# Optimization experiments

Hardware: AMD Instinct MI355X
Metric: run time of the kernel (lower is better)

The kernel has to match this reference:

```python
import jax, jax.numpy as jnp
import numpy as np

SHAPES = ((80, 80), (40, 40), (20, 20), (10, 10))  # (H, W) per level
N_HEADS = 8
N_POINTS = 4
D_MODEL = 512  # double_d_model = 2*256 (densefusion=True)
D_FFN = 1024
B = 2
L = len(SHAPES)
S = sum(h * w for h, w in SHAPES)  # 8500
EPS = 1e-5


def _layernorm(x, g, b):
    m = jnp.mean(x, axis=-1, keepdims=True)
    v = jnp.mean((x - m) ** 2, axis=-1, keepdims=True)
    return (x - m) * jax.lax.rsqrt(v + EPS) * g + b


def _reference_points(shapes):
    # encoder get_reference_points with valid_ratios == 1 -> [S, 2] (x, y) in (0,1)
    refs = []
    for (H, W) in shapes:
        ry = (jnp.arange(H, dtype=jnp.float32) + 0.5) / H
        rx = (jnp.arange(W, dtype=jnp.float32) + 0.5) / W
        gy, gx = jnp.meshgrid(ry, rx, indexing='ij')
        refs.append(jnp.stack([gx.reshape(-1), gy.reshape(-1)], axis=-1))
    return jnp.concatenate(refs, axis=0)


def _sample_level(val, loc, H, W):
    # val: [B, H*W, h, d]; loc: [B, S, h, P, 2] normalized in [0,1]
    b, _, h, d = val.shape
    s, p = loc.shape[1], loc.shape[3]
    x = loc[..., 0] * W - 0.5
    y = loc[..., 1] * H - 0.5
    x0 = jnp.floor(x)
    y0 = jnp.floor(y)
    wx = x - x0
    wy = y - y0
    x0i = x0.astype(jnp.int32)
    y0i = y0.astype(jnp.int32)

    def gather(xi, yi):
        valid = ((xi >= 0) & (xi < W) & (yi >= 0) & (yi < H)).astype(val.dtype)
        idx = jnp.clip(yi, 0, H - 1) * W + jnp.clip(xi, 0, W - 1)  # [B,S,h,P]
        idx2 = jnp.transpose(idx, (0, 1, 3, 2)).reshape(b, s * p, h)  # [B,S*P,h]
        g = jnp.take_along_axis(val, idx2[..., None], axis=1)  # [B,S*P,h,d]
        vmask = jnp.transpose(valid, (0, 1, 3, 2))[..., None]  # [B,S,P,h,1]
        return g.reshape(b, s, p, h, d) * vmask

    v00 = gather(x0i, y0i)
    v01 = gather(x0i + 1, y0i)
    v10 = gather(x0i, y0i + 1)
    v11 = gather(x0i + 1, y0i + 1)
    wxT = jnp.transpose(wx, (0, 1, 3, 2))[..., None]
    wyT = jnp.transpose(wy, (0, 1, 3, 2))[..., None]
    return (v00 * (1 - wxT) * (1 - wyT) + v01 * wxT * (1 - wyT)
            + v10 * (1 - wxT) * wyT + v11 * wxT * wyT)  # [B,S,P,h,d]


def _forward(src, pos, w_off, b_off, w_attn, b_attn, w_val, b_val, w_out, b_out,
             ln1_g, ln1_b, w1, b1, w2, b2, ln2_g, ln2_b, shapes):
    b, s, c = src.shape
    h, p, l = N_HEADS, N_POINTS, len(shapes)
    d = c // h
    q = src + pos
    value = (src @ w_val + b_val).reshape(b, s, h, d)
    offsets = (q @ w_off + b_off).reshape(b, s, h, l, p, 2)
    attn = jax.nn.softmax((q @ w_attn + b_attn).reshape(b, s, h, l * p), axis=-1)
    attn = attn.reshape(b, s, h, l, p)
    ref = _reference_points(shapes)  # [S,2]
    # offset normalizer = (W_l, H_l)
    norm = jnp.array([[W, H] for (H, W) in shapes], dtype=src.dtype)  # [L,2]
    loc = ref[None, :, None, None, None, :] + offsets / norm[None, None, None, :, None, :]
    # split value per level and sample
    starts = np.cumsum([0] + [H * W for (H, W) in shapes])[:-1]
    sampled = []
    for lvl, (H, W) in enumerate(shapes):
        val_l = jax.lax.dynamic_slice_in_dim(value, int(starts[lvl]), H * W, axis=1)
        sampled.append(_sample_level(val_l, loc[:, :, :, lvl], H, W))
    sampled = jnp.stack(sampled)  # [L,B,S,P,h,d]
    out = jnp.einsum('lbqphd,bqhlp->bqhd', sampled, attn).reshape(b, s, c)
    attn_out = out @ w_out + b_out
    x = _layernorm(src + attn_out, ln1_g, ln1_b)
    ffn = jax.nn.relu(x @ w1 + b1) @ w2 + b2
    return _layernorm(x + ffn, ln2_g, ln2_b)


def setup_inputs() -> dict:
    key = jax.random.key(0)
    ks = jax.random.split(key, 20)
    sc = 0.02
    C = D_MODEL
    hLP = N_HEADS * L * N_POINTS
    f32 = jnp.float32
    inp = {
        'src': jax.random.normal(ks[0], (B, S, C), f32),
        'pos': jax.random.normal(ks[1], (B, S, C), f32),
        'w_off': jax.random.normal(ks[2], (C, hLP * 2), f32) * sc,
        'b_off': jax.random.normal(ks[3], (hLP * 2,), f32) * sc,
        'w_attn': jax.random.normal(ks[4], (C, hLP), f32) * sc,
        'b_attn': jax.random.normal(ks[5], (hLP,), f32) * sc,
        'w_val': jax.random.normal(ks[6], (C, C), f32) * sc,
        'b_val': jnp.zeros((C,), f32),
        'w_out': jax.random.normal(ks[7], (C, C), f32) * sc,
        'b_out': jnp.zeros((C,), f32),
        'ln1_g': jnp.ones((C,), f32),
        'ln1_b': jnp.zeros((C,), f32),
        'w1': jax.random.normal(ks[8], (C, D_FFN), f32) * sc,
        'b1': jnp.zeros((D_FFN,), f32),
        'w2': jax.random.normal(ks[9], (D_FFN, C), f32) * sc,
        'b2': jnp.zeros((C,), f32),
        'ln2_g': jnp.ones((C,), f32),
        'ln2_b': jnp.zeros((C,), f32),
        'spatial_shapes': jnp.array(SHAPES, dtype=jnp.int32),
    }
    return inp


def reference(src, pos, w_off, b_off, w_attn, b_attn, w_val, b_val, w_out, b_out,
              ln1_g, ln1_b, w1, b1, w2, b2, ln2_g, ln2_b, spatial_shapes):
    shapes = tuple((int(a), int(b)) for a, b in np.asarray(spatial_shapes))
    return _forward(src, pos, w_off, b_off, w_attn, b_attn, w_val, b_val, w_out, b_out,
                    ln1_g, ln1_b, w1, b1, w2, b2, ln2_g, ln2_b, shapes)
```

## Files before the change

kernel.cpp:

```cpp
#include <hip/hip_runtime.h>


typedef __bf16 bf16_t;
typedef __bf16 bf16x8 __attribute__((ext_vector_type(8)));
typedef __bf16 bf16x4 __attribute__((ext_vector_type(4)));
typedef float  f32x2  __attribute__((ext_vector_type(2)));
typedef float  f32x4  __attribute__((ext_vector_type(4)));
typedef float  f32x16 __attribute__((ext_vector_type(16)));

#define M_ROWS 17000
#define S_LEN  8500

__device__ inline void store_c(float* p, float v)  { *p = v; }
__device__ inline void store_c(bf16_t* p, float v) { *p = (bf16_t)v; }

__device__ inline float4 load4f(const float* p)  { return *(const float4*)p; }
__device__ inline float4 load4f(const bf16_t* p) {
    bf16x4 v = *(const bf16x4*)p;
    return make_float4((float)v[0], (float)v[1], (float)v[2], (float)v[3]);
}

__device__ inline void pk_fma(f32x2& a, f32x2 x, f32x2 y) {
    asm("v_pk_fma_f32 %0, %1, %2, %0" : "+v"(a) : "v"(x), "v"(y));
}

__global__ __launch_bounds__(256)
void prep_kernel(const float* __restrict__ w_val, const float* __restrict__ w_off,
                 const float* __restrict__ w_attn, const float* __restrict__ w_out,
                 const float* __restrict__ w1, const float* __restrict__ w2,
                 const float* __restrict__ b_off, const float* __restrict__ b_attn,
                 bf16_t* __restrict__ wt_val, bf16_t* __restrict__ wt_oa,
                 bf16_t* __restrict__ wt_out, bf16_t* __restrict__ wt_w1,
                 bf16_t* __restrict__ wt_w2, float* __restrict__ bias_oa) {
    int z = blockIdx.z;
    if (z == 6) {
        if (blockIdx.x == 0 && blockIdx.y == 0) {
            for (int i = threadIdx.x; i < 384; i += 256)
                bias_oa[i] = (i < 256) ? b_off[i] : b_attn[i - 256];
        }
        return;
    }
    const float* in; bf16_t* out; int K, N;
    switch (z) {
        case 0: in = w_val;  out = wt_val;                     K = 512;  N = 512;  break;
        case 1: in = w_off;  out = wt_oa;                      K = 512;  N = 256;  break;
        case 2: in = w_attn; out = wt_oa + (size_t)256 * 512;  K = 512;  N = 128;  break;
        case 3: in = w_out;  out = wt_out;                     K = 512;  N = 512;  break;
        case 4: in = w1;     out = wt_w1;                      K = 512;  N = 1024; break;
        default: in = w2;    out = wt_w2;                      K = 1024; N = 512;  break;
    }
    int k0 = blockIdx.x * 32, n0 = blockIdx.y * 32;
    if (k0 >= K || n0 >= N) return;
    __shared__ float s[32][33];
    int tx = threadIdx.x & 31, ty = threadIdx.x >> 5;
    #pragma unroll
    for (int i = 0; i < 4; i++)
        s[ty + 8 * i][tx] = in[(size_t)(k0 + ty + 8 * i) * N + n0 + tx];
    __syncthreads();
    #pragma unroll
    for (int i = 0; i < 4; i++)
        out[(size_t)(n0 + ty + 8 * i) * K + k0 + tx] = (bf16_t)s[tx][ty + 8 * i];
}

__global__ __launch_bounds__(256)
void add_q_kernel(const float* __restrict__ a, const float* __restrict__ b,
                  bf16_t* __restrict__ q, bf16_t* __restrict__ src_bf, int n4) {
    int i = blockIdx.x * 256 + threadIdx.x;
    if (i >= n4) return;
    float4 av = *(const float4*)(a + (size_t)i * 4);
    float4 bv = *(const float4*)(b + (size_t)i * 4);
    bf16x4 sv, ov;
    sv[0] = (bf16_t)av.x; sv[1] = (bf16_t)av.y; sv[2] = (bf16_t)av.z; sv[3] = (bf16_t)av.w;
    ov[0] = (bf16_t)(av.x + bv.x);
    ov[1] = (bf16_t)(av.y + bv.y);
    ov[2] = (bf16_t)(av.z + bv.z);
    ov[3] = (bf16_t)(av.w + bv.w);
    *(bf16x4*)(q      + (size_t)i * 4) = ov;
    *(bf16x4*)(src_bf + (size_t)i * 4) = sv;
}

#define GEMM_CORE(A_PTR, WT_PTR, K_DIM, EPILOGUE)                                  \
    const int tid  = threadIdx.x;                                                  \
    const int wave = tid >> 6;                                                     \
    const int lane = tid & 63;                                                     \
    const int l31  = lane & 31;                                                    \
    const int lh8  = (lane >> 5) * 8;                                              \
    const int wr   = (wave >> 1) * 64;                                             \
    const int wc   = (wave & 1) * 64;                                              \
    const int row0 = blockIdx.x * 128;                                             \
    const int sr = tid >> 2;                                                       \
    const int sc = (tid & 3) * 8;                                                  \
    const bf16_t* gA0 = A_PTR  + (size_t)min(row0 + sr,      M_ROWS - 1) * K_DIM + sc; \
    const bf16_t* gA1 = A_PTR  + (size_t)min(row0 + sr + 64, M_ROWS - 1) * K_DIM + sc; \
    const bf16_t* gB0 = WT_PTR + (size_t)(col0 + sr) * K_DIM + sc;                 \
    const bf16_t* gB1 = WT_PTR + (size_t)(col0 + sr + 64) * K_DIM + sc;            \
    f32x16 acc[2][2];                                                              \
    _Pragma("unroll")                                                              \
    for (int i = 0; i < 2; i++)                                                    \
        _Pragma("unroll")                                                          \
        for (int j = 0; j < 2; j++)                                                \
            _Pragma("unroll")                                                      \
            for (int r = 0; r < 16; r++) acc[i][j][r] = 0.f;                       \
    bf16x8 pa0 = *(const bf16x8*)gA0;                                              \
    bf16x8 pa1 = *(const bf16x8*)gA1;                                              \
    bf16x8 pb0 = *(const bf16x8*)gB0;                                              \
    bf16x8 pb1 = *(const bf16x8*)gB1;                                              \
    const int nIter = K_DIM >> 5;                                                  \
    for (int it = 0; it < nIter; it++) {                                           \
        const int cur = it & 1;                                                    \
        *(bf16x8*)&As[cur][sr][sc]      = pa0;                                     \
        *(bf16x8*)&As[cur][sr + 64][sc] = pa1;                                     \
        *(bf16x8*)&Bs[cur][sr][sc]      = pb0;                                     \
        *(bf16x8*)&Bs[cur][sr + 64][sc] = pb1;                                     \
        __syncthreads();                                                           \
        if (it + 1 < nIter) {                                                      \
            int ko = (it + 1) << 5;                                                \
            pa0 = *(const bf16x8*)(gA0 + ko);                                      \
            pa1 = *(const bf16x8*)(gA1 + ko);                                      \
            pb0 = *(const bf16x8*)(gB0 + ko);                                      \
            pb1 = *(const bf16x8*)(gB1 + ko);                                      \
        }                                                                          \
        _Pragma("unroll")                                                          \
        for (int kh = 0; kh < 2; kh++) {                                           \
            bf16x8 a0 = *(const bf16x8*)&As[cur][wr + l31     ][kh * 16 + lh8];    \
            bf16x8 a1 = *(const bf16x8*)&As[cur][wr + 32 + l31][kh * 16 + lh8];    \
            bf16x8 b0 = *(const bf16x8*)&Bs[cur][wc + l31     ][kh * 16 + lh8];    \
            bf16x8 b1 = *(const bf16x8*)&Bs[cur][wc + 32 + l31][kh * 16 + lh8];    \
            acc[0][0] = __builtin_amdgcn_mfma_f32_32x32x16_bf16(a0, b0, acc[0][0], 0, 0, 0); \
            acc[0][1] = __builtin_amdgcn_mfma_f32_32x32x16_bf16(a0, b1, acc[0][1], 0, 0, 0); \
            acc[1][0] = __builtin_amdgcn_mfma_f32_32x32x16_bf16(a1, b0, acc[1][0], 0, 0, 0); \
            acc[1][1] = __builtin_amdgcn_mfma_f32_32x32x16_bf16(a1, b1, acc[1][1], 0, 0, 0); \
        }                                                                          \
    }                                                                              \
    EPILOGUE

template<typename OT, bool RELU>
__global__ __launch_bounds__(256)
void gemm128_kernel(const bf16_t* __restrict__ A, const bf16_t* __restrict__ Wt,
                    const float* __restrict__ bias, OT* __restrict__ Cout,
                    int N, int K) {
    __shared__ bf16_t As[2][128][40];
    __shared__ bf16_t Bs[2][128][40];
    const int col0 = blockIdx.y * 128;
    GEMM_CORE(A, Wt, K,
        {
            _Pragma("unroll")
            for (int i = 0; i < 2; i++)
                _Pragma("unroll")
                for (int j = 0; j < 2; j++) {
                    int col = col0 + wc + j * 32 + l31;
                    float bcol = bias[col];
                    _Pragma("unroll")
                    for (int reg = 0; reg < 16; reg++) {
                        int row = row0 + wr + i * 32 + (reg & 3) + 8 * (reg >> 2) + 4 * (lane >> 5);
                        if (row < M_ROWS) {
                            float v = acc[i][j][reg] + bcol;
                            if (RELU) v = fmaxf(v, 0.f);
                            store_c(Cout + (size_t)row * N + col, v);
                        }
                    }
                }
        }
    )
}

__global__ __launch_bounds__(256)
void gemm_voa_kernel(const bf16_t* __restrict__ src_bf, const bf16_t* __restrict__ q,
                     const bf16_t* __restrict__ wt_val, const bf16_t* __restrict__ wt_oa,
                     const float* __restrict__ b_val, const float* __restrict__ bias_oa,
                     bf16_t* __restrict__ value, float* __restrict__ oa) {
    __shared__ bf16_t As[2][128][40];
    __shared__ bf16_t Bs[2][128][40];
    const int by    = blockIdx.y;
    const bool isV  = by < 4;
    const int col0  = (isV ? by : by - 4) * 128;
    const bf16_t* Ap  = isV ? src_bf : q;
    const bf16_t* Wp  = isV ? wt_val : wt_oa;
    const float* bp   = isV ? b_val : bias_oa;
    GEMM_CORE(Ap, Wp, 512,
        {
            _Pragma("unroll")
            for (int i = 0; i < 2; i++)
                _Pragma("unroll")
                for (int j = 0; j < 2; j++) {
                    int col = col0 + wc + j * 32 + l31;
                    float bcol = bp[col];
                    _Pragma("unroll")
                    for (int reg = 0; reg < 16; reg++) {
                        int row = row0 + wr + i * 32 + (reg & 3) + 8 * (reg >> 2) + 4 * (lane >> 5);
                        if (row < M_ROWS) {
                            float v = acc[i][j][reg] + bcol;
                            if (isV) value[(size_t)row * 512 + col] = (bf16_t)v;
                            else     oa[(size_t)row * 384 + col] = v;
                        }
                    }
                }
        }
    )
}

__global__ __launch_bounds__(256)
void sample_kernel(const bf16_t* __restrict__ value, const float* __restrict__ oa,
                   bf16_t* __restrict__ out) {
    __shared__ __align__(16) int sAW[4][2][8][68];
    const int wave = threadIdx.x >> 6;
    const int lane = threadIdx.x & 63;
    const int h    = lane >> 3;
    const int sub  = lane & 7;
    const int bs   = blockIdx.x * 4 + wave;
    const int b    = bs / S_LEN;
    const int s    = bs - b * S_LEN;

    float rx, ry;
    if (s < 6400)      { int i = s;        const float inv = 1.f/80.f; ry = ((i/80) + 0.5f)*inv; rx = ((i%80) + 0.5f)*inv; }
    else if (s < 8000) { int i = s - 6400; const float inv = 1.f/40.f; ry = ((i/40) + 0.5f)*inv; rx = ((i%40) + 0.5f)*inv; }
    else if (s < 8400) { int i = s - 8000; const float inv = 1.f/20.f; ry = ((i/20) + 0.5f)*inv; rx = ((i%20) + 0.5f)*inv; }
    else               { int i = s - 8400; const float inv = 1.f/10.f; ry = ((i/10) + 0.5f)*inv; rx = ((i%10) + 0.5f)*inv; }

    const int WH[4]  = {80, 40, 20, 10};
    const int LST[4] = {0, 6400, 8000, 8400};
    const int ll = sub >> 1;
    const int W  = WH[ll];
    const int LS = LST[ll];

    const float* row = oa + (size_t)bs * 384;
    float4 o4 = *(const float4*)(row + h * 32 + sub * 4);
    float2 lg = *(const float2*)(row + 256 + h * 16 + sub * 2);

    float mx = fmaxf(lg.x, lg.y);
    mx = fmaxf(mx, __shfl_xor(mx, 1, 64));
    mx = fmaxf(mx, __shfl_xor(mx, 2, 64));
    mx = fmaxf(mx, __shfl_xor(mx, 4, 64));
    float e0 = __expf(lg.x - mx), e1 = __expf(lg.y - mx);
    float sm = e0 + e1;
    sm += __shfl_xor(sm, 1, 64);
    sm += __shfl_xor(sm, 2, 64);
    sm += __shfl_xor(sm, 4, 64);
    float pinv = 1.f / sm;

    #pragma unroll
    for (int t = 0; t < 2; t++) {
        float ox = t ? o4.z : o4.x;
        float oy = t ? o4.w : o4.y;
        float p  = (t ? e1 : e0) * pinv;
        float x = fmaf(rx, (float)W, ox) - 0.5f;
        float y = fmaf(ry, (float)W, oy) - 0.5f;
        float fx = floorf(x), fy = floorf(y);
        float wx = x - fx, wy = y - fy;
        int ix = (int)fx, iy = (int)fy;
        #pragma unroll
        for (int k2 = 0; k2 < 4; k2++) {
            int cx = ix + (k2 & 1);
            int cy = iy + (k2 >> 1);
            float wgt = p * ((k2 & 1) ? wx : 1.f - wx) * ((k2 >> 1) ? wy : 1.f - wy);
            if (cx < 0 || cx >= W || cy < 0 || cy >= W) wgt = 0.f;
            int xc = min(max(cx, 0), W - 1);
            int yc = min(max(cy, 0), W - 1);
            int c = sub * 8 + t * 4 + k2;
            sAW[wave][0][h][c] = LS + yc * W + xc;
            sAW[wave][1][h][c] = __float_as_int(wgt);
        }
    }
    __syncthreads();

    const bf16_t* vb = value + ((size_t)b * S_LEN) * 512 + h * 64 + sub * 8;
    f32x2 a01 = {0.f, 0.f}, a23 = {0.f, 0.f}, a45 = {0.f, 0.f}, a67 = {0.f, 0.f};

    #define ACC8(V, WW) {                                                          \
        f32x2 ws; ws[0] = (WW); ws[1] = (WW);                                      \
        f32x2 pv;                                                                  \
        pv[0] = __uint_as_float((V).x << 16);                                      \
        pv[1] = __uint_as_float((V).x & 0xffff0000u); pk_fma(a01, pv, ws);         \
        pv[0] = __uint_as_float((V).y << 16);                                      \
        pv[1] = __uint_as_float((V).y & 0xffff0000u); pk_fma(a23, pv, ws);         \
        pv[0] = __uint_as_float((V).z << 16);                                      \
        pv[1] = __uint_as_float((V).z & 0xffff0000u); pk_fma(a45, pv, ws);         \
        pv[0] = __uint_as_float((V).w << 16);                                      \
        pv[1] = __uint_as_float((V).w & 0xffff0000u); pk_fma(a67, pv, ws); }

    #pragma unroll 2
    for (int c8 = 0; c8 < 64; c8 += 8) {
        int4   ia = *(const int4*)  &sAW[wave][0][h][c8];
        int4   ib = *(const int4*)  &sAW[wave][0][h][c8 + 4];
        float4 wa = *(const float4*)&sAW[wave][1][h][c8];
        float4 wb = *(const float4*)&sAW[wave][1][h][c8 + 4];
        uint4 v0 = *(const uint4*)(vb + (size_t)ia.x * 512);
        uint4 v1 = *(const uint4*)(vb + (size_t)ia.y * 512);
        uint4 v2 = *(const uint4*)(vb + (size_t)ia.z * 512);
        uint4 v3 = *(const uint4*)(vb + (size_t)ia.w * 512);
        uint4 v4 = *(const uint4*)(vb + (size_t)ib.x * 512);
        uint4 v5 = *(const uint4*)(vb + (size_t)ib.y * 512);
        uint4 v6 = *(const uint4*)(vb + (size_t)ib.z * 512);
        uint4 v7 = *(const uint4*)(vb + (size_t)ib.w * 512);
        ACC8(v0, wa.x) ACC8(v1, wa.y) ACC8(v2, wa.z) ACC8(v3, wa.w)
        ACC8(v4, wb.x) ACC8(v5, wb.y) ACC8(v6, wb.z) ACC8(v7, wb.w)
    }
    #undef ACC8

    bf16x8 ov;
    ov[0] = (bf16_t)a01[0]; ov[1] = (bf16_t)a01[1];
    ov[2] = (bf16_t)a23[0]; ov[3] = (bf16_t)a23[1];
    ov[4] = (bf16_t)a45[0]; ov[5] = (bf16_t)a45[1];
    ov[6] = (bf16_t)a67[0]; ov[7] = (bf16_t)a67[1];
    *(bf16x8*)(out + (size_t)bs * 512 + h * 64 + sub * 8) = ov;
}

template<typename INA, typename INB, typename OT>
__global__ __launch_bounds__(256)
void ln_kernel(const INA* __restrict__ Xa, const INB* __restrict__ Xb,
               const float* __restrict__ g, const float* __restrict__ be,
               OT* __restrict__ out, int M) {
    int wave = threadIdx.x >> 6;
    int lane = threadIdx.x & 63;
    int row = blockIdx.x * 4 + wave;
    if (row >= M) return;
    size_t base = (size_t)row * 512;
    float v[8];
    float s = 0.f, sq = 0.f;
    #pragma unroll
    for (int p = 0; p < 2; p++) {
        int idx = p * 256 + lane * 4;
        float4 a4 = load4f(Xa + base + idx);
        float4 b4 = load4f(Xb + base + idx);
        float t0 = a4.x + b4.x, t1 = a4.y + b4.y, t2 = a4.z + b4.z, t3 = a4.w + b4.w;
        v[p*4+0] = t0; v[p*4+1] = t1; v[p*4+2] = t2; v[p*4+3] = t3;
        s  += t0 + t1 + t2 + t3;
        sq += t0*t0 + t1*t1 + t2*t2 + t3*t3;
    }
    #pragma unroll
    for (int off = 32; off > 0; off >>= 1) {
        s  += __shfl_xor(s, off, 64);
        sq += __shfl_xor(sq, off, 64);
    }
    float mean = s * (1.f / 512.f);
    float var  = sq * (1.f / 512.f) - mean * mean;
    float rstd = rsqrtf(var + 1e-5f);
    #pragma unroll
    for (int p = 0; p < 2; p++) {
        int idx = p * 256 + lane * 4;
        #pragma unroll
        for (int j = 0; j < 4; j++) {
            int col = idx + j;
            float o = (v[p*4+j] - mean) * rstd * g[col] + be[col];
            store_c(out + base + col, o);
        }
    }
}

extern "C" void kernel_launch(void* const* d_in, const int* in_sizes, int n_in,
                              void* d_out, int out_size, void* d_ws, size_t ws_size,
                              hipStream_t stream) {
    const float* src    = (const float*)d_in[0];
    const float* pos    = (const float*)d_in[1];
    const float* w_off  = (const float*)d_in[2];
    const float* b_off  = (const float*)d_in[3];
    const float* w_attn = (const float*)d_in[4];
    const float* b_attn = (const float*)d_in[5];
    const float* w_val  = (const float*)d_in[6];
    const float* b_val  = (const float*)d_in[7];
    const float* w_out  = (const float*)d_in[8];
    const float* b_out  = (const float*)d_in[9];
    const float* ln1_g  = (const float*)d_in[10];
    const float* ln1_b  = (const float*)d_in[11];
    const float* w1     = (const float*)d_in[12];
    const float* b1     = (const float*)d_in[13];
    const float* w2     = (const float*)d_in[14];
    const float* b2     = (const float*)d_in[15];
    const float* ln2_g  = (const float*)d_in[16];
    const float* ln2_b  = (const float*)d_in[17];

    const int M = M_ROWS;
    char* ws = (char*)d_ws;
    size_t o = 0;
    auto alloc = [&](size_t bytes) { size_t r = o; o += (bytes + 255) & ~(size_t)255; return r; };

    size_t off_q       = alloc((size_t)M * 512 * 2);
    size_t off_srcbf   = alloc((size_t)M * 512 * 2);
    size_t off_value   = alloc((size_t)M * 512 * 2);
    size_t off_sampled = alloc((size_t)M * 512 * 2);
    size_t off_oa      = alloc((size_t)M * 384 * 4);
    size_t off_attnout = alloc((size_t)M * 512 * 2);
    size_t off_x       = alloc((size_t)M * 512 * 2);
    size_t off_wtval   = alloc((size_t)512 * 512 * 2);
    size_t off_wtoa    = alloc((size_t)384 * 512 * 2);
    size_t off_wtout   = alloc((size_t)512 * 512 * 2);
    size_t off_wtw1    = alloc((size_t)1024 * 512 * 2);
    size_t off_wtw2    = alloc((size_t)512 * 1024 * 2);
    size_t off_boa     = alloc((size_t)384 * 4);

    bf16_t* q        = (bf16_t*)(ws + off_q);
    bf16_t* src_bf   = (bf16_t*)(ws + off_srcbf);
    bf16_t* value    = (bf16_t*)(ws + off_value);
    bf16_t* sampled  = (bf16_t*)(ws + off_sampled);
    float*  oa       = (float*)(ws + off_oa);
    bf16_t* attn_out = (bf16_t*)(ws + off_attnout);
    bf16_t* x        = (bf16_t*)(ws + off_x);
    bf16_t* hidden   = (bf16_t*)(ws + off_sampled);
    bf16_t* ffn_out  = (bf16_t*)(ws + off_attnout);
    bf16_t* wt_val   = (bf16_t*)(ws + off_wtval);
    bf16_t* wt_oa    = (bf16_t*)(ws + off_wtoa);
    bf16_t* wt_out   = (bf16_t*)(ws + off_wtout);
    bf16_t* wt_w1    = (bf16_t*)(ws + off_wtw1);
    bf16_t* wt_w2    = (bf16_t*)(ws + off_wtw2);
    float*  bias_oa  = (float*)(ws + off_boa);
    float*  outp     = (float*)d_out;

    prep_kernel<<<dim3(32, 32, 7), 256, 0, stream>>>(
        w_val, w_off, w_attn, w_out, w1, w2, b_off, b_attn,
        wt_val, wt_oa, wt_out, wt_w1, wt_w2, bias_oa);

    add_q_kernel<<<(M * 512 / 4 + 255) / 256, 256, 0, stream>>>(src, pos, q, src_bf, M * 512 / 4);

    const int MT = (M + 127) / 128;

    gemm_voa_kernel<<<dim3(MT, 7), 256, 0, stream>>>(src_bf, q, wt_val, wt_oa, b_val, bias_oa, value, oa);

    sample_kernel<<<M / 4, 256, 0, stream>>>(value, oa, sampled);

    gemm128_kernel<bf16_t, false><<<dim3(MT, 4), 256, 0, stream>>>(sampled, wt_out, b_out, attn_out, 512, 512);

    ln_kernel<float, bf16_t, bf16_t><<<(M + 3) / 4, 256, 0, stream>>>(src, attn_out, ln1_g, ln1_b, x, M);

    gemm128_kernel<bf16_t, true ><<<dim3(MT, 8), 256, 0, stream>>>(x, wt_w1, b1, hidden, 1024, 512);
    gemm128_kernel<bf16_t, false><<<dim3(MT, 4), 256, 0, stream>>>(hidden, wt_w2, b2, ffn_out, 512, 1024);

    ln_kernel<bf16_t, bf16_t, float><<<(M + 3) / 4, 256, 0, stream>>>(x, ffn_out, ln2_g, ln2_b, outp, M);
}
```

Measured before the change: 358.3 us.

## Swizzle workgroups across XCDs and unroll GEMM K-loop with deeper prefetch

Adds an XCD-aware remapping of the flat workgroup index so that consecutive tiles land on the same XCD. This is applied to the GEMMs and the sampling kernel, with the aim of improving L2 reuse of shared A/B rows and value data. The GEMM main loop is unrolled by two, with two register prefetch sets and fixed LDS buffer indices. K becomes a template constant so the loop count is known at compile time. The risks are higher register pressure and a swizzle that may not help on kernels that are mainly streaming.

```diff
diff --git a/kernel.cpp b/kernel.cpp
--- a/kernel.cpp
+++ b/kernel.cpp
@@ -22,6 +22,14 @@
 
 __device__ inline void pk_fma(f32x2& a, f32x2 x, f32x2 y) {
     asm("v_pk_fma_f32 %0, %1, %2, %0" : "+v"(a) : "v"(x), "v"(y));
+}
+
+__device__ inline int swz_flat() {
+    int o   = blockIdx.x + gridDim.x * blockIdx.y;
+    int nwg = gridDim.x * gridDim.y;
+    int q = nwg >> 3, r = nwg & 7;
+    int xcd = o & 7, s = o >> 3;
+    return (xcd < r ? xcd * (q + 1) : r * (q + 1) + (xcd - r) * q) + s;
 }
 
 __global__ __launch_bounds__(256)
@@ -79,6 +87,19 @@
     *(bf16x4*)(src_bf + (size_t)i * 4) = sv;
 }
 
+#define MMA_PHASE(CUR)                                                             \
+    _Pragma("unroll")                                                              \
+    for (int kh = 0; kh < 2; kh++) {                                               \
+        bf16x8 a0 = *(const bf16x8*)&As[CUR][wr + l31     ][kh * 16 + lh8];        \
+        bf16x8 a1 = *(const bf16x8*)&As[CUR][wr + 32 + l31][kh * 16 + lh8];        \
+        bf16x8 b0 = *(const bf16x8*)&Bs[CUR][wc + l31     ][kh * 16 + lh8];        \
+        bf16x8 b1 = *(const bf16x8*)&Bs[CUR][wc + 32 + l31][kh * 16 + lh8];        \
+        acc[0][0] = __builtin_amdgcn_mfma_f32_32x32x16_bf16(a0, b0, acc[0][0], 0, 0, 0); \
+        acc[0][1] = __builtin_amdgcn_mfma_f32_32x32x16_bf16(a0, b1, acc[0][1], 0, 0, 0); \
+        acc[1][0] = __builtin_amdgcn_mfma_f32_32x32x16_bf16(a1, b0, acc[1][0], 0, 0, 0); \
+        acc[1][1] = __builtin_amdgcn_mfma_f32_32x32x16_bf16(a1, b1, acc[1][1], 0, 0, 0); \
+    }
+
 #define GEMM_CORE(A_PTR, WT_PTR, K_DIM, EPILOGUE)                                  \
     const int tid  = threadIdx.x;                                                  \
     const int wave = tid >> 6;                                                     \
@@ -87,13 +108,12 @@
     const int lh8  = (lane >> 5) * 8;                                              \
     const int wr   = (wave >> 1) * 64;                                             \
     const int wc   = (wave & 1) * 64;                                              \
-    const int row0 = blockIdx.x * 128;                                             \
     const int sr = tid >> 2;                                                       \
     const int sc = (tid & 3) * 8;                                                  \
-    const bf16_t* gA0 = A_PTR  + (size_t)min(row0 + sr,      M_ROWS - 1) * K_DIM + sc; \
-    const bf16_t* gA1 = A_PTR  + (size_t)min(row0 + sr + 64, M_ROWS - 1) * K_DIM + sc; \
-    const bf16_t* gB0 = WT_PTR + (size_t)(col0 + sr) * K_DIM + sc;                 \
-    const bf16_t* gB1 = WT_PTR + (size_t)(col0 + sr + 64) * K_DIM + sc;            \
+    const bf16_t* gA0 = A_PTR  + (size_t)min(row0 + sr,      M_ROWS - 1) * (K_DIM) + sc; \
+    const bf16_t* gA1 = A_PTR  + (size_t)min(row0 + sr + 64, M_ROWS - 1) * (K_DIM) + sc; \
+    const bf16_t* gB0 = WT_PTR + (size_t)(col0 + sr) * (K_DIM) + sc;               \
+    const bf16_t* gB1 = WT_PTR + (size_t)(col0 + sr + 64) * (K_DIM) + sc;          \
     f32x16 acc[2][2];                                                              \
     _Pragma("unroll")                                                              \
     for (int i = 0; i < 2; i++)                                                    \
@@ -101,48 +121,56 @@
         for (int j = 0; j < 2; j++)                                                \
             _Pragma("unroll")                                                      \
             for (int r = 0; r < 16; r++) acc[i][j][r] = 0.f;                       \
-    bf16x8 pa0 = *(const bf16x8*)gA0;                                              \
-    bf16x8 pa1 = *(const bf16x8*)gA1;                                              \
-    bf16x8 pb0 = *(const bf16x8*)gB0;                                              \
-    bf16x8 pb1 = *(const bf16x8*)gB1;                                              \
-    const int nIter = K_DIM >> 5;                                                  \
-    for (int it = 0; it < nIter; it++) {                                           \
-        const int cur = it & 1;                                                    \
-        *(bf16x8*)&As[cur][sr][sc]      = pa0;                                     \
-        *(bf16x8*)&As[cur][sr + 64][sc] = pa1;                                     \
-        *(bf16x8*)&Bs[cur][sr][sc]      = pb0;                                     \
-        *(bf16x8*)&Bs[cur][sr + 64][sc] = pb1;                                     \
+    bf16x8 paA0 = *(const bf16x8*)gA0;                                             \
+    bf16x8 paA1 = *(const bf16x8*)gA1;                                             \
+    bf16x8 pbA0 = *(const bf16x8*)gB0;                                             \
+    bf16x8 pbA1 = *(const bf16x8*)gB1;                                             \
+    bf16x8 paB0 = *(const bf16x8*)(gA0 + 32);                                      \
+    bf16x8 paB1 = *(const bf16x8*)(gA1 + 32);                                      \
+    bf16x8 pbB0 = *(const bf16x8*)(gB0 + 32);                                      \
+    bf16x8 pbB1 = *(const bf16x8*)(gB1 + 32);                                      \
+    const int nIter = (K_DIM) >> 5;                                                \
+    for (int it = 0; it < nIter; it += 2) {                                        \
+        *(bf16x8*)&As[0][sr][sc]      = paA0;                                      \
+        *(bf16x8*)&As[0][sr + 64][sc] = paA1;                                      \
+        *(bf16x8*)&Bs[0][sr][sc]      = pbA0;                                      \
+        *(bf16x8*)&Bs[0][sr + 64][sc] = pbA1;                                      \
         __syncthreads();                                                           \
-        if (it + 1 < nIter) {                                                      \
-            int ko = (it + 1) << 5;                                                \
-            pa0 = *(const bf16x8*)(gA0 + ko);                                      \
-            pa1 = *(const bf16x8*)(gA1 + ko);                                      \
-            pb0 = *(const bf16x8*)(gB0 + ko);                                      \
-            pb1 = *(const bf16x8*)(gB1 + ko);                                      \
+        if (it + 2 < nIter) {                                                      \
+            const int ko = (it + 2) << 5;                                          \
+            paA0 = *(const bf16x8*)(gA0 + ko);                                     \
+            paA1 = *(const bf16x8*)(gA1 + ko);                                     \
+            pbA0 = *(const bf16x8*)(gB0 + ko);                                     \
+            pbA1 = *(const bf16x8*)(gB1 + ko);                                     \
         }                                                                          \
-        _Pragma("unroll")                                                          \
-        for (int kh = 0; kh < 2; kh++) {                                           \
-            bf16x8 a0 = *(const bf16x8*)&As[cur][wr + l31     ][kh * 16 + lh8];    \
-            bf16x8 a1 = *(const bf16x8*)&As[cur][wr + 32 + l31][kh * 16 + lh8];    \
-            bf16x8 b0 = *(const bf16x8*)&Bs[cur][wc + l31     ][kh * 16 + lh8];    \
-            bf16x8 b1 = *(const bf16x8*)&Bs[cur][wc + 32 + l31][kh * 16 + lh8];    \
-            acc[0][0] = __builtin_amdgcn_mfma_f32_32x32x16_bf16(a0, b0, acc[0][0], 0, 0, 0); \
-            acc[0][1] = __builtin_amdgcn_mfma_f32_32x32x16_bf16(a0, b1, acc[0][1], 0, 0, 0); \
-            acc[1][0] = __builtin_amdgcn_mfma_f32_32x32x16_bf16(a1, b0, acc[1][0], 0, 0, 0); \
-            acc[1][1] = __builtin_amdgcn_mfma_f32_32x32x16_bf16(a1, b1, acc[1][1], 0, 0, 0); \
+        MMA_PHASE(0)                                                               \
+        *(bf16x8*)&As[1][sr][sc]      = paB0;                                      \
+        *(bf16x8*)&As[1][sr + 64][sc] = paB1;                                      \
+        *(bf16x8*)&Bs[1][sr][sc]      = pbB0;                                      \
+        *(bf16x8*)&Bs[1][sr + 64][sc] = pbB1;                                      \
+        __syncthreads();                                                           \
+        if (it + 3 < nIter) {                                                      \
+            const int ko = (it + 3) << 5;                                          \
+            paB0 = *(const bf16x8*)(gA0 + ko);                                     \
+            paB1 = *(const bf16x8*)(gA1 + ko);                                     \
+            pbB0 = *(const bf16x8*)(gB0 + ko);                                     \
+            pbB1 = *(const bf16x8*)(gB1 + ko);                                     \
         }                                                                          \
+        MMA_PHASE(1)                                                               \
     }                                                                              \
     EPILOGUE
 
-template<typename OT, bool RELU>
+template<typename OT, bool RELU, int KD>
 __global__ __launch_bounds__(256)
 void gemm128_kernel(const bf16_t* __restrict__ A, const bf16_t* __restrict__ Wt,
-                    const float* __restrict__ bias, OT* __restrict__ Cout,
-                    int N, int K) {
+                    const float* __restrict__ bias, OT* __restrict__ Cout, int N) {
     __shared__ bf16_t As[2][128][40];
     __shared__ bf16_t Bs[2][128][40];
-    const int col0 = blockIdx.y * 128;
-    GEMM_CORE(A, Wt, K,
+    const int wg = swz_flat();
+    const int NY = gridDim.y;
+    const int row0 = (wg / NY) * 128;
+    const int col0 = (wg % NY) * 128;
+    GEMM_CORE(A, Wt, KD,
         {
             _Pragma("unroll")
             for (int i = 0; i < 2; i++)
@@ -171,9 +199,11 @@
                      bf16_t* __restrict__ value, float* __restrict__ oa) {
     __shared__ bf16_t As[2][128][40];
     __shared__ bf16_t Bs[2][128][40];
-    const int by    = blockIdx.y;
+    const int wg = swz_flat();
+    const int by = wg % 7;
     const bool isV  = by < 4;
     const int col0  = (isV ? by : by - 4) * 128;
+    const int row0  = (wg / 7) * 128;
     const bf16_t* Ap  = isV ? src_bf : q;
     const bf16_t* Wp  = isV ? wt_val : wt_oa;
     const float* bp   = isV ? b_val : bias_oa;
@@ -207,7 +237,7 @@
     const int lane = threadIdx.x & 63;
     const int h    = lane >> 3;
     const int sub  = lane & 7;
-    const int bs   = blockIdx.x * 4 + wave;
+    const int bs   = swz_flat() * 4 + wave;
     const int b    = bs / S_LEN;
     const int s    = bs - b * S_LEN;
 
@@ -417,12 +447,12 @@
 
     sample_kernel<<<M / 4, 256, 0, stream>>>(value, oa, sampled);
 
-    gemm128_kernel<bf16_t, false><<<dim3(MT, 4), 256, 0, stream>>>(sampled, wt_out, b_out, attn_out, 512, 512);
+    gemm128_kernel<bf16_t, false, 512><<<dim3(MT, 4), 256, 0, stream>>>(sampled, wt_out, b_out, attn_out, 512);
 
     ln_kernel<float, bf16_t, bf16_t><<<(M + 3) / 4, 256, 0, stream>>>(src, attn_out, ln1_g, ln1_b, x, M);
 
-    gemm128_kernel<bf16_t, true ><<<dim3(MT, 8), 256, 0, stream>>>(x, wt_w1, b1, hidden, 1024, 512);
-    gemm128_kernel<bf16_t, false><<<dim3(MT, 4), 256, 0, stream>>>(hidden, wt_w2, b2, ffn_out, 512, 1024);
+    gemm128_kernel<bf16_t, true, 512 ><<<dim3(MT, 8), 256, 0, stream>>>(x, wt_w1, b1, hidden, 1024);
+    gemm128_kernel<bf16_t, false, 1024><<<dim3(MT, 4), 256, 0, stream>>>(hidden, wt_w2, b2, ffn_out, 512);
 
     ln_kernel<bf16_t, bf16_t, float><<<(M + 3) / 4, 256, 0, stream>>>(x, ffn_out, ln2_g, ln2_b, outp, M);
 }
```

After: 364.0 us. Within noise of the previous version (+1.6%).

## Add 128x64 GEMM tiles, XCD-aware block swizzle, and compile-time K

Applied to the files above, without the earlier changes.

Adds a 128x64-tile GEMM variant and uses it for the value/offset-attention projection, the output projection and the second FFN GEMM. This doubles the workgroup count so more of the 256 CUs are occupied on M=17000. Also adds an XCD-aware workgroup remapping so consecutive tiles that share A rows land on the same XCD for L2 reuse, applied to the GEMMs and the sampling kernel. K becomes a template parameter. The smaller tiles add more A-tile reloads and lower MFMA density per wave.

```diff
diff --git a/kernel.cpp b/kernel.cpp
--- a/kernel.cpp
+++ b/kernel.cpp
@@ -22,6 +22,14 @@
 
 __device__ inline void pk_fma(f32x2& a, f32x2 x, f32x2 y) {
     asm("v_pk_fma_f32 %0, %1, %2, %0" : "+v"(a) : "v"(x), "v"(y));
+}
+
+__device__ inline int swz_flat() {
+    int o   = blockIdx.x + gridDim.x * blockIdx.y;
+    int nwg = gridDim.x * gridDim.y;
+    int q = nwg >> 3, r = nwg & 7;
+    int xcd = o & 7, s = o >> 3;
+    return (xcd < r ? xcd * (q + 1) : r * (q + 1) + (xcd - r) * q) + s;
 }
 
 __global__ __launch_bounds__(256)
@@ -87,13 +95,12 @@
     const int lh8  = (lane >> 5) * 8;                                              \
     const int wr   = (wave >> 1) * 64;                                             \
     const int wc   = (wave & 1) * 64;                                              \
-    const int row0 = blockIdx.x * 128;                                             \
     const int sr = tid >> 2;                                                       \
     const int sc = (tid & 3) * 8;                                                  \
-    const bf16_t* gA0 = A_PTR  + (size_t)min(row0 + sr,      M_ROWS - 1) * K_DIM + sc; \
-    const bf16_t* gA1 = A_PTR  + (size_t)min(row0 + sr + 64, M_ROWS - 1) * K_DIM + sc; \
-    const bf16_t* gB0 = WT_PTR + (size_t)(col0 + sr) * K_DIM + sc;                 \
-    const bf16_t* gB1 = WT_PTR + (size_t)(col0 + sr + 64) * K_DIM + sc;            \
+    const bf16_t* gA0 = A_PTR  + (size_t)min(row0 + sr,      M_ROWS - 1) * (K_DIM) + sc; \
+    const bf16_t* gA1 = A_PTR  + (size_t)min(row0 + sr + 64, M_ROWS - 1) * (K_DIM) + sc; \
+    const bf16_t* gB0 = WT_PTR + (size_t)(col0 + sr) * (K_DIM) + sc;               \
+    const bf16_t* gB1 = WT_PTR + (size_t)(col0 + sr + 64) * (K_DIM) + sc;          \
     f32x16 acc[2][2];                                                              \
     _Pragma("unroll")                                                              \
     for (int i = 0; i < 2; i++)                                                    \
@@ -105,7 +112,7 @@
     bf16x8 pa1 = *(const bf16x8*)gA1;                                              \
     bf16x8 pb0 = *(const bf16x8*)gB0;                                              \
     bf16x8 pb1 = *(const bf16x8*)gB1;                                              \
-    const int nIter = K_DIM >> 5;                                                  \
+    const int nIter = (K_DIM) >> 5;                                                \
     for (int it = 0; it < nIter; it++) {                                           \
         const int cur = it & 1;                                                    \
         *(bf16x8*)&As[cur][sr][sc]      = pa0;                                     \
@@ -134,15 +141,61 @@
     }                                                                              \
     EPILOGUE
 
-template<typename OT, bool RELU>
+#define GEMM64_CORE(A_PTR, WT_PTR, K_DIM, EPILOGUE)                                \
+    const int tid  = threadIdx.x;                                                  \
+    const int wave = tid >> 6;                                                     \
+    const int lane = tid & 63;                                                     \
+    const int l31  = lane & 31;                                                    \
+    const int lh8  = (lane >> 5) * 8;                                              \
+    const int wr   = wave * 32;                                                    \
+    const int sr = tid >> 2;                                                       \
+    const int sc = (tid & 3) * 8;                                                  \
+    const bf16_t* gA0 = A_PTR  + (size_t)min(row0 + sr,      M_ROWS - 1) * (K_DIM) + sc; \
+    const bf16_t* gA1 = A_PTR  + (size_t)min(row0 + sr + 64, M_ROWS - 1) * (K_DIM) + sc; \
+    const bf16_t* gB0 = WT_PTR + (size_t)(col0 + sr) * (K_DIM) + sc;               \
+    f32x16 acc[2];                                                                 \
+    _Pragma("unroll")                                                              \
+    for (int j = 0; j < 2; j++)                                                    \
+        _Pragma("unroll")                                                          \
+        for (int r = 0; r < 16; r++) acc[j][r] = 0.f;                              \
+    bf16x8 pa0 = *(const bf16x8*)gA0;                                              \
+    bf16x8 pa1 = *(const bf16x8*)gA1;                                              \
+    bf16x8 pb0 = *(const bf16x8*)gB0;                                              \
+    const int nIter = (K_DIM) >> 5;                                                \
+    for (int it = 0; it < nIter; it++) {                                           \
+        const int cur = it & 1;                                                    \
+        *(bf16x8*)&As[cur][sr][sc]      = pa0;                                     \
+        *(bf16x8*)&As[cur][sr + 64][sc] = pa1;                                     \
+        *(bf16x8*)&Bs[cur][sr][sc]      = pb0;                                     \
+        __syncthreads();                                                           \
+        if (it + 1 < nIter) {                                                      \
+            int ko = (it + 1) << 5;                                                \
+            pa0 = *(const bf16x8*)(gA0 + ko);                                      \
+            pa1 = *(const bf16x8*)(gA1 + ko);                                      \
+            pb0 = *(const bf16x8*)(gB0 + ko);                                      \
+        }                                                                          \
+        _Pragma("unroll")                                                          \
+        for (int kh = 0; kh < 2; kh++) {                                           \
+            bf16x8 a0 = *(const bf16x8*)&As[cur][wr + l31][kh * 16 + lh8];         \
+            bf16x8 b0 = *(const bf16x8*)&Bs[cur][l31     ][kh * 16 + lh8];         \
+            bf16x8 b1 = *(const bf16x8*)&Bs[cur][32 + l31][kh * 16 + lh8];         \
+            acc[0] = __builtin_amdgcn_mfma_f32_32x32x16_bf16(a0, b0, acc[0], 0, 0, 0); \
+            acc[1] = __builtin_amdgcn_mfma_f32_32x32x16_bf16(a0, b1, acc[1], 0, 0, 0); \
+        }                                                                          \
+    }                                                                              \
+    EPILOGUE
+
+template<typename OT, bool RELU, int KD>
 __global__ __launch_bounds__(256)
 void gemm128_kernel(const bf16_t* __restrict__ A, const bf16_t* __restrict__ Wt,
-                    const float* __restrict__ bias, OT* __restrict__ Cout,
-                    int N, int K) {
+                    const float* __restrict__ bias, OT* __restrict__ Cout, int N) {
     __shared__ bf16_t As[2][128][40];
     __shared__ bf16_t Bs[2][128][40];
-    const int col0 = blockIdx.y * 128;
-    GEMM_CORE(A, Wt, K,
+    const int wg = swz_flat();
+    const int NY = gridDim.y;
+    const int row0 = (wg / NY) * 128;
+    const int col0 = (wg % NY) * 128;
+    GEMM_CORE(A, Wt, KD,
         {
             _Pragma("unroll")
             for (int i = 0; i < 2; i++)
@@ -164,37 +217,67 @@
     )
 }
 
+template<typename OT, bool RELU, int KD>
+__global__ __launch_bounds__(256)
+void gemm64_kernel(const bf16_t* __restrict__ A, const bf16_t* __restrict__ Wt,
+                   const float* __restrict__ bias, OT* __restrict__ Cout, int N) {
+    __shared__ bf16_t As[2][128][40];
+    __shared__ bf16_t Bs[2][64][40];
+    const int wg = swz_flat();
+    const int NY = gridDim.y;
+    const int row0 = (wg / NY) * 128;
+    const int col0 = (wg % NY) * 64;
+    GEMM64_CORE(A, Wt, KD,
+        {
+            _Pragma("unroll")
+            for (int j = 0; j < 2; j++) {
+                int col = col0 + j * 32 + l31;
+                float bcol = bias[col];
+                _Pragma("unroll")
+                for (int reg = 0; reg < 16; reg++) {
+                    int row = row0 + wr + (reg & 3) + 8 * (reg >> 2) + 4 * (lane >> 5);
+                    if (row < M_ROWS) {
+                        float v = acc[j][reg] + bcol;
+                        if (RELU) v = fmaxf(v, 0.f);
+                        store_c(Cout + (size_t)row * N + col, v);
+                    }
+                }
+            }
+        }
+    )
+}
+
 __global__ __launch_bounds__(256)
 void gemm_voa_kernel(const bf16_t* __restrict__ src_bf, const bf16_t* __restrict__ q,
                      const bf16_t* __restrict__ wt_val, const bf16_t* __restrict__ wt_oa,
                      const float* __restrict__ b_val, const float* __restrict__ bias_oa,
                      bf16_t* __restrict__ value, float* __restrict__ oa) {
     __shared__ bf16_t As[2][128][40];
-    __shared__ bf16_t Bs[2][128][40];
-    const int by    = blockIdx.y;
-    const bool isV  = by < 4;
-    const int col0  = (isV ? by : by - 4) * 128;
+    __shared__ bf16_t Bs[2][64][40];
+    const int wg = swz_flat();
+    const int by = wg % 14;
+    const bool isV  = by < 8;
+    const int col0  = (isV ? by : by - 8) * 64;
+    const int row0  = (wg / 14) * 128;
     const bf16_t* Ap  = isV ? src_bf : q;
     const bf16_t* Wp  = isV ? wt_val : wt_oa;
     const float* bp   = isV ? b_val : bias_oa;
-    GEMM_CORE(Ap, Wp, 512,
+    GEMM64_CORE(Ap, Wp, 512,
         {
             _Pragma("unroll")
-            for (int i = 0; i < 2; i++)
+            for (int j = 0; j < 2; j++) {
+                int col = col0 + j * 32 + l31;
+                float bcol = bp[col];
                 _Pragma("unroll")
-                for (int j = 0; j < 2; j++) {
-                    int col = col0 + wc + j * 32 + l31;
-                    float bcol = bp[col];
-                    _Pragma("unroll")
-                    for (int reg = 0; reg < 16; reg++) {
-                        int row = row0 + wr + i * 32 + (reg & 3) + 8 * (reg >> 2) + 4 * (lane >> 5);
-                        if (row < M_ROWS) {
-                            float v = acc[i][j][reg] + bcol;
-                            if (isV) value[(size_t)row * 512 + col] = (bf16_t)v;
-                            else     oa[(size_t)row * 384 + col] = v;
-                        }
+                for (int reg = 0; reg < 16; reg++) {
+                    int row = row0 + wr + (reg & 3) + 8 * (reg >> 2) + 4 * (lane >> 5);
+                    if (row < M_ROWS) {
+                        float v = acc[j][reg] + bcol;
+                        if (isV) value[(size_t)row * 512 + col] = (bf16_t)v;
+                        else     oa[(size_t)row * 384 + col] = v;
                     }
                 }
+            }
         }
     )
 }
@@ -207,7 +290,7 @@
     const int lane = threadIdx.x & 63;
     const int h    = lane >> 3;
     const int sub  = lane & 7;
-    const int bs   = blockIdx.x * 4 + wave;
+    const int bs   = swz_flat() * 4 + wave;
     const int b    = bs / S_LEN;
     const int s    = bs - b * S_LEN;
 
@@ -413,16 +496,16 @@
 
     const int MT = (M + 127) / 128;
 
-    gemm_voa_kernel<<<dim3(MT, 7), 256, 0, stream>>>(src_bf, q, wt_val, wt_oa, b_val, bias_oa, value, oa);
+    gemm_voa_kernel<<<dim3(MT, 14), 256, 0, stream>>>(src_bf, q, wt_val, wt_oa, b_val, bias_oa, value, oa);
 
     sample_kernel<<<M / 4, 256, 0, stream>>>(value, oa, sampled);
 
-    gemm128_kernel<bf16_t, false><<<dim3(MT, 4), 256, 0, stream>>>(sampled, wt_out, b_out, attn_out, 512, 512);
+    gemm64_kernel<bf16_t, false, 512><<<dim3(MT, 8), 256, 0, stream>>>(sampled, wt_out, b_out, attn_out, 512);
 
     ln_kernel<float, bf16_t, bf16_t><<<(M + 3) / 4, 256, 0, stream>>>(src, attn_out, ln1_g, ln1_b, x, M);
 
-    gemm128_kernel<bf16_t, true ><<<dim3(MT, 8), 256, 0, stream>>>(x, wt_w1, b1, hidden, 1024, 512);
-    gemm128_kernel<bf16_t, false><<<dim3(MT, 4), 256, 0, stream>>>(hidden, wt_w2, b2, ffn_out, 512, 1024);
+    gemm128_kernel<bf16_t, true, 512><<<dim3(MT, 8), 256, 0, stream>>>(x, wt_w1, b1, hidden, 1024);
+    gemm64_kernel<bf16_t, false, 1024><<<dim3(MT, 8), 256, 0, stream>>>(hidden, wt_w2, b2, ffn_out, 512);
 
     ln_kernel<bf16_t, bf16_t, float><<<(M + 3) / 4, 256, 0, stream>>>(x, ffn_out, ln2_g, ln2_b, outp, M);
 }
```

After: 358.5 us. About the same (+0.0%).

## Replace LDS-tiled GEMMs with register-resident weight GEMMs and XCD-aware block swizzle

Applied to the files above, without the earlier changes.

All GEMMs drop the shared-memory double-buffered 128x128 tiles. Each wave now holds a full 32-column weight slice for the whole K dimension in registers and streams A rows straight from global memory over four 32-row tiles. The K=1024 FFN down-projection splits K across wave pairs and reduces through LDS. A block-index swizzle groups consecutive work onto the same XCD for L2 locality, and the sampling kernel uses it too. This trades LDS reuse of A for heavy register pressure and uncached A reads from global memory, which each wave reads separately.

```diff
diff --git a/kernel.cpp b/kernel.cpp
--- a/kernel.cpp
+++ b/kernel.cpp
@@ -22,6 +22,14 @@
 
 __device__ inline void pk_fma(f32x2& a, f32x2 x, f32x2 y) {
     asm("v_pk_fma_f32 %0, %1, %2, %0" : "+v"(a) : "v"(x), "v"(y));
+}
+
+__device__ inline int swz_flat() {
+    int o   = blockIdx.x + gridDim.x * blockIdx.y;
+    int nwg = gridDim.x * gridDim.y;
+    int q = nwg >> 3, r = nwg & 7;
+    int xcd = o & 7, s = o >> 3;
+    return (xcd < r ? xcd * (q + 1) : r * (q + 1) + (xcd - r) * q) + s;
 }
 
 __global__ __launch_bounds__(256)
@@ -79,124 +87,151 @@
     *(bf16x4*)(src_bf + (size_t)i * 4) = sv;
 }
 
-#define GEMM_CORE(A_PTR, WT_PTR, K_DIM, EPILOGUE)                                  \
-    const int tid  = threadIdx.x;                                                  \
-    const int wave = tid >> 6;                                                     \
-    const int lane = tid & 63;                                                     \
-    const int l31  = lane & 31;                                                    \
-    const int lh8  = (lane >> 5) * 8;                                              \
-    const int wr   = (wave >> 1) * 64;                                             \
-    const int wc   = (wave & 1) * 64;                                              \
-    const int row0 = blockIdx.x * 128;                                             \
-    const int sr = tid >> 2;                                                       \
-    const int sc = (tid & 3) * 8;                                                  \
-    const bf16_t* gA0 = A_PTR  + (size_t)min(row0 + sr,      M_ROWS - 1) * K_DIM + sc; \
-    const bf16_t* gA1 = A_PTR  + (size_t)min(row0 + sr + 64, M_ROWS - 1) * K_DIM + sc; \
-    const bf16_t* gB0 = WT_PTR + (size_t)(col0 + sr) * K_DIM + sc;                 \
-    const bf16_t* gB1 = WT_PTR + (size_t)(col0 + sr + 64) * K_DIM + sc;            \
-    f32x16 acc[2][2];                                                              \
-    _Pragma("unroll")                                                              \
-    for (int i = 0; i < 2; i++)                                                    \
-        _Pragma("unroll")                                                          \
-        for (int j = 0; j < 2; j++)                                                \
-            _Pragma("unroll")                                                      \
-            for (int r = 0; r < 16; r++) acc[i][j][r] = 0.f;                       \
-    bf16x8 pa0 = *(const bf16x8*)gA0;                                              \
-    bf16x8 pa1 = *(const bf16x8*)gA1;                                              \
-    bf16x8 pb0 = *(const bf16x8*)gB0;                                              \
-    bf16x8 pb1 = *(const bf16x8*)gB1;                                              \
-    const int nIter = K_DIM >> 5;                                                  \
-    for (int it = 0; it < nIter; it++) {                                           \
-        const int cur = it & 1;                                                    \
-        *(bf16x8*)&As[cur][sr][sc]      = pa0;                                     \
-        *(bf16x8*)&As[cur][sr + 64][sc] = pa1;                                     \
-        *(bf16x8*)&Bs[cur][sr][sc]      = pb0;                                     \
-        *(bf16x8*)&Bs[cur][sr + 64][sc] = pb1;                                     \
-        __syncthreads();                                                           \
-        if (it + 1 < nIter) {                                                      \
-            int ko = (it + 1) << 5;                                                \
-            pa0 = *(const bf16x8*)(gA0 + ko);                                      \
-            pa1 = *(const bf16x8*)(gA1 + ko);                                      \
-            pb0 = *(const bf16x8*)(gB0 + ko);                                      \
-            pb1 = *(const bf16x8*)(gB1 + ko);                                      \
-        }                                                                          \
-        _Pragma("unroll")                                                          \
-        for (int kh = 0; kh < 2; kh++) {                                           \
-            bf16x8 a0 = *(const bf16x8*)&As[cur][wr + l31     ][kh * 16 + lh8];    \
-            bf16x8 a1 = *(const bf16x8*)&As[cur][wr + 32 + l31][kh * 16 + lh8];    \
-            bf16x8 b0 = *(const bf16x8*)&Bs[cur][wc + l31     ][kh * 16 + lh8];    \
-            bf16x8 b1 = *(const bf16x8*)&Bs[cur][wc + 32 + l31][kh * 16 + lh8];    \
-            acc[0][0] = __builtin_amdgcn_mfma_f32_32x32x16_bf16(a0, b0, acc[0][0], 0, 0, 0); \
-            acc[0][1] = __builtin_amdgcn_mfma_f32_32x32x16_bf16(a0, b1, acc[0][1], 0, 0, 0); \
-            acc[1][0] = __builtin_amdgcn_mfma_f32_32x32x16_bf16(a1, b0, acc[1][0], 0, 0, 0); \
-            acc[1][1] = __builtin_amdgcn_mfma_f32_32x32x16_bf16(a1, b1, acc[1][1], 0, 0, 0); \
-        }                                                                          \
-    }                                                                              \
-    EPILOGUE
-
-template<typename OT, bool RELU>
-__global__ __launch_bounds__(256)
-void gemm128_kernel(const bf16_t* __restrict__ A, const bf16_t* __restrict__ Wt,
-                    const float* __restrict__ bias, OT* __restrict__ Cout,
-                    int N, int K) {
-    __shared__ bf16_t As[2][128][40];
-    __shared__ bf16_t Bs[2][128][40];
-    const int col0 = blockIdx.y * 128;
-    GEMM_CORE(A, Wt, K,
-        {
-            _Pragma("unroll")
-            for (int i = 0; i < 2; i++)
-                _Pragma("unroll")
-                for (int j = 0; j < 2; j++) {
-                    int col = col0 + wc + j * 32 + l31;
-                    float bcol = bias[col];
-                    _Pragma("unroll")
-                    for (int reg = 0; reg < 16; reg++) {
-                        int row = row0 + wr + i * 32 + (reg & 3) + 8 * (reg >> 2) + 4 * (lane >> 5);
-                        if (row < M_ROWS) {
-                            float v = acc[i][j][reg] + bcol;
-                            if (RELU) v = fmaxf(v, 0.f);
-                            store_c(Cout + (size_t)row * N + col, v);
-                        }
-                    }
+
+template<typename OT, bool RELU, int KD>
+__global__ __launch_bounds__(256, 2)
+void gemm_breg_kernel(const bf16_t* __restrict__ A, const bf16_t* __restrict__ Wt,
+                      const float* __restrict__ bias, OT* __restrict__ Cout, int N) {
+    const int lane = threadIdx.x & 63;
+    const int wave = threadIdx.x >> 6;
+    const int l31  = lane & 31;
+    const int pl   = lane >> 5;
+    const int CG   = gridDim.x;
+    const int wg   = swz_flat();
+    const int bx   = wg % CG;
+    const int by   = wg / CG;
+    const int cb   = (bx * 4 + wave) * 32;
+
+    const bf16_t* bp = Wt + (size_t)(cb + l31) * KD + pl * 8;
+    bf16x8 b[KD / 16];
+    #pragma unroll
+    for (int ks = 0; ks < KD / 16; ks++) b[ks] = *(const bf16x8*)(bp + ks * 16);
+    const float bcol = bias[cb + l31];
+
+    #pragma unroll 1
+    for (int j = 0; j < 4; j++) {
+        const int r0 = (by * 4 + j) * 32;
+        const bf16_t* ap = A + (size_t)min(r0 + l31, M_ROWS - 1) * KD + pl * 8;
+        f32x16 acc;
+        #pragma unroll
+        for (int r = 0; r < 16; r++) acc[r] = 0.f;
+        #pragma unroll
+        for (int ks = 0; ks < KD / 16; ks++) {
+            bf16x8 a = *(const bf16x8*)(ap + ks * 16);
+            acc = __builtin_amdgcn_mfma_f32_32x32x16_bf16(a, b[ks], acc, 0, 0, 0);
+        }
+        #pragma unroll
+        for (int reg = 0; reg < 16; reg++) {
+            int row = r0 + (reg & 3) + 8 * (reg >> 2) + 4 * pl;
+            if (row < M_ROWS) {
+                float v = acc[reg] + bcol;
+                if (RELU) v = fmaxf(v, 0.f);
+                store_c(Cout + (size_t)row * N + cb + l31, v);
+            }
+        }
+    }
+}
+
+__global__ __launch_bounds__(256, 2)
+void gemm_voa_breg_kernel(const bf16_t* __restrict__ src_bf, const bf16_t* __restrict__ q,
+                          const bf16_t* __restrict__ wt_val, const bf16_t* __restrict__ wt_oa,
+                          const float* __restrict__ b_val, const float* __restrict__ bias_oa,
+                          bf16_t* __restrict__ value, float* __restrict__ oa) {
+    const int lane = threadIdx.x & 63;
+    const int wave = threadIdx.x >> 6;
+    const int l31  = lane & 31;
+    const int pl   = lane >> 5;
+    const int wg   = swz_flat();
+    const int bx   = wg % 7;
+    const int by   = wg / 7;
+    const int cbi  = bx * 4 + wave;
+    const bool isV = cbi < 16;
+    const int colb = (isV ? cbi : cbi - 16) * 32;
+    const bf16_t* Ap = isV ? src_bf : q;
+    const bf16_t* Wp = isV ? wt_val : wt_oa;
+    const float bcol = (isV ? b_val : bias_oa)[colb + l31];
+
+    const bf16_t* bp = Wp + (size_t)(colb + l31) * 512 + pl * 8;
+    bf16x8 b[32];
+    #pragma unroll
+    for (int ks = 0; ks < 32; ks++) b[ks] = *(const bf16x8*)(bp + ks * 16);
+
+    #pragma unroll 1
+    for (int j = 0; j < 4; j++) {
+        const int r0 = (by * 4 + j) * 32;
+        const bf16_t* ap = Ap + (size_t)min(r0 + l31, M_ROWS - 1) * 512 + pl * 8;
+        f32x16 acc;
+        #pragma unroll
+        for (int r = 0; r < 16; r++) acc[r] = 0.f;
+        #pragma unroll
+        for (int ks = 0; ks < 32; ks++) {
+            bf16x8 a = *(const bf16x8*)(ap + ks * 16);
+            acc = __builtin_amdgcn_mfma_f32_32x32x16_bf16(a, b[ks], acc, 0, 0, 0);
+        }
+        #pragma unroll
+        for (int reg = 0; reg < 16; reg++) {
+            int row = r0 + (reg & 3) + 8 * (reg >> 2) + 4 * pl;
+            if (row < M_ROWS) {
+                float v = acc[reg] + bcol;
+                if (isV) value[(size_t)row * 512 + colb + l31] = (bf16_t)v;
+                else     oa[(size_t)row * 384 + colb + l31] = v;
+            }
+        }
+    }
+}
+
+__global__ __launch_bounds__(256, 2)
+void gemm_breg_ks_kernel(const bf16_t* __restrict__ A, const bf16_t* __restrict__ Wt,
+                         const float* __restrict__ bias, bf16_t* __restrict__ Cout) {
+    __shared__ float red[2][64][16];
+    const int lane = threadIdx.x & 63;
+    const int wave = threadIdx.x >> 6;
+    const int l31  = lane & 31;
+    const int pl   = lane >> 5;
+    const int cb2  = wave >> 1;
+    const int kh2  = wave & 1;
+    const int wg   = swz_flat();
+    const int bx   = wg % 8;
+    const int by   = wg / 8;
+    const int cb   = (bx * 2 + cb2) * 32;
+
+    const bf16_t* bp = Wt + (size_t)(cb + l31) * 1024 + kh2 * 512 + pl * 8;
+    bf16x8 b[32];
+    #pragma unroll
+    for (int ks = 0; ks < 32; ks++) b[ks] = *(const bf16x8*)(bp + ks * 16);
+    const float bcol = bias[cb + l31];
+
+    #pragma unroll 1
+    for (int j = 0; j < 4; j++) {
+        const int r0 = (by * 4 + j) * 32;
+        const bf16_t* ap = A + (size_t)min(r0 + l31, M_ROWS - 1) * 1024 + kh2 * 512 + pl * 8;
+        f32x16 acc;
+        #pragma unroll
+        for (int r = 0; r < 16; r++) acc[r] = 0.f;
+        #pragma unroll
+        for (int ks = 0; ks < 32; ks++) {
+            bf16x8 a = *(const bf16x8*)(ap + ks * 16);
+            acc = __builtin_amdgcn_mfma_f32_32x32x16_bf16(a, b[ks], acc, 0, 0, 0);
+        }
+        if (kh2) {
+            #pragma unroll
+            for (int r4 = 0; r4 < 4; r4++)
+                *(f32x4*)&red[cb2][lane][r4 * 4] =
+                    f32x4{acc[r4*4], acc[r4*4+1], acc[r4*4+2], acc[r4*4+3]};
+        }
+        __syncthreads();
+        if (!kh2) {
+            #pragma unroll
+            for (int reg = 0; reg < 16; reg++) {
+                int row = r0 + (reg & 3) + 8 * (reg >> 2) + 4 * pl;
+                if (row < M_ROWS) {
+                    float v = acc[reg] + red[cb2][lane][reg] + bcol;
+                    Cout[(size_t)row * 512 + cb + l31] = (bf16_t)v;
                 }
-        }
-    )
-}
-
-__global__ __launch_bounds__(256)
-void gemm_voa_kernel(const bf16_t* __restrict__ src_bf, const bf16_t* __restrict__ q,
-                     const bf16_t* __restrict__ wt_val, const bf16_t* __restrict__ wt_oa,
-                     const float* __restrict__ b_val, const float* __restrict__ bias_oa,
-                     bf16_t* __restrict__ value, float* __restrict__ oa) {
-    __shared__ bf16_t As[2][128][40];
-    __shared__ bf16_t Bs[2][128][40];
-    const int by    = blockIdx.y;
-    const bool isV  = by < 4;
-    const int col0  = (isV ? by : by - 4) * 128;
-    const bf16_t* Ap  = isV ? src_bf : q;
-    const bf16_t* Wp  = isV ? wt_val : wt_oa;
-    const float* bp   = isV ? b_val : bias_oa;
-    GEMM_CORE(Ap, Wp, 512,
-        {
-            _Pragma("unroll")
-            for (int i = 0; i < 2; i++)
-                _Pragma("unroll")
-                for (int j = 0; j < 2; j++) {
-                    int col = col0 + wc + j * 32 + l31;
-                    float bcol = bp[col];
-                    _Pragma("unroll")
-                    for (int reg = 0; reg < 16; reg++) {
-                        int row = row0 + wr + i * 32 + (reg & 3) + 8 * (reg >> 2) + 4 * (lane >> 5);
-                        if (row < M_ROWS) {
-                            float v = acc[i][j][reg] + bcol;
-                            if (isV) value[(size_t)row * 512 + col] = (bf16_t)v;
-                            else     oa[(size_t)row * 384 + col] = v;
-                        }
-                    }
-                }
-        }
-    )
+            }
+        }
+        __syncthreads();
+    }
 }
 
 __global__ __launch_bounds__(256)
@@ -207,7 +242,7 @@
     const int lane = threadIdx.x & 63;
     const int h    = lane >> 3;
     const int sub  = lane & 7;
-    const int bs   = blockIdx.x * 4 + wave;
+    const int bs   = swz_flat() * 4 + wave;
     const int b    = bs / S_LEN;
     const int s    = bs - b * S_LEN;
 
@@ -411,18 +446,22 @@
 
     add_q_kernel<<<(M * 512 / 4 + 255) / 256, 256, 0, stream>>>(src, pos, q, src_bf, M * 512 / 4);
 
-    const int MT = (M + 127) / 128;
-
-    gemm_voa_kernel<<<dim3(MT, 7), 256, 0, stream>>>(src_bf, q, wt_val, wt_oa, b_val, bias_oa, value, oa);
+    const int RG = 133;
+
+    gemm_voa_breg_kernel<<<dim3(7, RG), 256, 0, stream>>>(
+        src_bf, q, wt_val, wt_oa, b_val, bias_oa, value, oa);
 
     sample_kernel<<<M / 4, 256, 0, stream>>>(value, oa, sampled);
 
-    gemm128_kernel<bf16_t, false><<<dim3(MT, 4), 256, 0, stream>>>(sampled, wt_out, b_out, attn_out, 512, 512);
+    gemm_breg_kernel<bf16_t, false, 512><<<dim3(4, RG), 256, 0, stream>>>(
+        sampled, wt_out, b_out, attn_out, 512);
 
     ln_kernel<float, bf16_t, bf16_t><<<(M + 3) / 4, 256, 0, stream>>>(src, attn_out, ln1_g, ln1_b, x, M);
 
-    gemm128_kernel<bf16_t, true ><<<dim3(MT, 8), 256, 0, stream>>>(x, wt_w1, b1, hidden, 1024, 512);
-    gemm128_kernel<bf16_t, false><<<dim3(MT, 4), 256, 0, stream>>>(hidden, wt_w2, b2, ffn_out, 512, 1024);
+    gemm_breg_kernel<bf16_t, true, 512><<<dim3(8, RG), 256, 0, stream>>>(
+        x, wt_w1, b1, hidden, 1024);
+
+    gemm_breg_ks_kernel<<<dim3(8, RG), 256, 0, stream>>>(hidden, wt_w2, b2, ffn_out);
 
     ln_kernel<bf16_t, bf16_t, float><<<(M + 3) / 4, 256, 0, stream>>>(x, ffn_out, ln2_g, ln2_b, outp, M);
 }
```

Result: slower. 532.1 us (+48.5%).
